# Optimization experiments

Hardware: AMD Instinct MI355X
Metric: run time of the kernel (lower is better)

## Reference

```python
import jax, jax.numpy as jnp
import numpy as np

N = 100000      # nodes
E = 3200000     # edges
H = 64          # node_hidden_dim
DIN = 15        # node_input_dim
DOUT = 12       # output_dim
NT = 5          # num_edge_type
G = 256         # graphs in batch
STEPS = 6       # num_step_prop


def setup_inputs() -> dict:
    key = jax.random.key(0)
    ks = jax.random.split(key, 24)
    s = 0.1
    n = lambda k, shp: jax.random.normal(k, shp, jnp.float32) * s
    return {
        "x": jax.random.normal(ks[0], (N, DIN), jnp.float32),
        "edge_index": jax.random.randint(ks[1], (2, E), 0, N, dtype=jnp.int32),
        "edge_attr": jax.random.randint(ks[2], (E,), 0, NT, dtype=jnp.int32),
        "batch": jnp.sort(jax.random.randint(ks[3], (N,), 0, G, dtype=jnp.int32)),
        "lin0_w": n(ks[4], (DIN, H)), "lin0_b": n(ks[5], (H,)),
        "edge_embed": n(ks[6], (NT, H * H)),
        "conv_bias": n(ks[7], (H,)),
        "gru_w_ih": n(ks[8], (H, 3 * H)), "gru_w_hh": n(ks[9], (H, 3 * H)),
        "gru_b_ih": n(ks[10], (3 * H,)), "gru_b_hh": n(ks[11], (3 * H,)),
        "i_w1": n(ks[12], (2 * H, H)), "i_b1": n(ks[13], (H,)),
        "i_w2": n(ks[14], (H, DOUT)), "i_b2": n(ks[15], (DOUT,)),
        "j_w1": n(ks[16], (H, H)), "j_b1": n(ks[17], (H,)),
        "j_w2": n(ks[18], (H, DOUT)), "j_b2": n(ks[19], (DOUT,)),
    }


def reference(x, edge_index, edge_attr, batch,
              lin0_w, lin0_b, edge_embed, conv_bias,
              gru_w_ih, gru_w_hh, gru_b_ih, gru_b_hh,
              i_w1, i_b1, i_w2, i_b2, j_w1, j_b1, j_w2, j_b2):
    src, dst = edge_index[0], edge_index[1]
    W_types = edge_embed.reshape(NT, H, H)  # per edge-type [H_in, H_out]

    # in-degree for mean aggregation (PyG: isolated nodes get 0)
    deg = jax.ops.segment_sum(jnp.ones((E,), x.dtype), dst, num_segments=N)
    deg = jnp.maximum(deg, 1.0)[:, None]

    out0 = jax.nn.relu(x @ lin0_w + lin0_b)
    out = out0
    h = out0

    for _ in range(STEPS):
        # NNConv: per-edge matmul m_e = x_src[e] @ W[type_e].
        # Only NT=5 edge types exist -> precompute all 5 transforms, then gather.
        T = jnp.einsum('nh,tho->nto', out, W_types)        # [N, NT, H]
        msg = T[src, edge_attr]                            # [E, H] gather
        agg = jax.ops.segment_sum(msg, dst, num_segments=N) / deg + conv_bias
        m = jax.nn.relu(agg)

        # GRU cell (torch gate order: r, z, n)
        gx = m @ gru_w_ih + gru_b_ih
        gh = h @ gru_w_hh + gru_b_hh
        xr, xz, xn = jnp.split(gx, 3, axis=1)
        hr, hz, hn = jnp.split(gh, 3, axis=1)
        r = jax.nn.sigmoid(xr + hr)
        z = jax.nn.sigmoid(xz + hz)
        nn_ = jnp.tanh(xn + r * hn)
        h = (1.0 - z) * nn_ + z * h
        out = h

    # gated readout
    i = jax.nn.sigmoid(
        jax.nn.sigmoid(jnp.concatenate([out, out0], axis=1) @ i_w1 + i_b1) @ i_w2 + i_b2)
    j = jax.nn.sigmoid(out @ j_w1 + j_b1) @ j_w2 + j_b2
    gated = i * j                                          # [N, DOUT]
    return jax.ops.segment_sum(gated, batch, num_segments=G)  # [G, DOUT]
```

## Files before the change

kernel.cpp:

```cpp
#include <hip/hip_runtime.h>
#include <hip/hip_bf16.h>

typedef __hip_bfloat16 bf16;
using short8 = __attribute__((ext_vector_type(8))) short;
using f32x4  = __attribute__((ext_vector_type(4))) float;
using f32x2  = __attribute__((ext_vector_type(2))) float;

#define MFMA16(a,b,c) __builtin_amdgcn_mfma_f32_16x16x32_bf16((a),(b),(c),0,0,0)
#define MAXBUCK 4096
#define SB 72
#define MSTR 72
#define SRCCAP 1024

__device__ __forceinline__ float b2f(bf16 v){ return __bfloat162float(v); }
__device__ __forceinline__ bf16  f2b(float v){ return __float2bfloat16(v); }
__device__ __forceinline__ float sigmf(float x){ return 1.f/(1.f+__expf(-x)); }
__device__ __forceinline__ float tanhfast(float x){
  x = fminf(fmaxf(x,-15.f),15.f);
  float e = __expf(2.f*x);
  return (e-1.f)/(e+1.f);
}
__device__ __forceinline__ short8 ld_frag(const bf16* p){
  return *reinterpret_cast<const short8*>(p);
}
__device__ __forceinline__ short f2bits(float f){
  unsigned u = __builtin_bit_cast(unsigned, f);
  unsigned r = (u + 0x7FFFu + ((u>>16)&1u)) >> 16;
  return (short)r;
}
__device__ __forceinline__ f32x2 up2(unsigned w){
  f32x2 r;
  r.x = __builtin_bit_cast(float, w<<16);
  r.y = __builtin_bit_cast(float, w & 0xFFFF0000u);
  return r;
}
__device__ __forceinline__ f32x2 pk_add(f32x2 a, f32x2 b){
  f32x2 d;
  asm("v_pk_add_f32 %0, %1, %2" : "=v"(d) : "v"(a), "v"(b));
  return d;
}
__device__ __forceinline__ unsigned cvtpk_bf16(float lo, float hi){
  unsigned r;
  asm("v_cvt_pk_bf16_f32 %0, %1, %2" : "=v"(r) : "v"(lo), "v"(hi));
  return r;
}


__global__ void k_sniff(const unsigned int* __restrict__ x, int* __restrict__ flag){
  int t = threadIdx.x;
  int good = 0;
  for (int i=t; i<4096; i+=256){
    unsigned w = x[i];
    unsigned e = (w>>23)&0xFFu;
    unsigned m = w & 0x7FFFFFFFu;
    if ((e>=100u && e<=150u) || m==0u) good++;
  }
  __shared__ int sm[256];
  sm[t]=good; __syncthreads();
  if (t==0){ int s=0; for (int k=0;k<256;k++) s+=sm[k]; *flag = (s>2048)?1:0; }
}

struct PtrPack { const void* p[17]; };

#define CAN_X     0
#define CAN_L0W   1500032
#define CAN_L0B   1500992
#define CAN_EE    1501056
#define CAN_CB    1521536
#define CAN_WIH   1521600
#define CAN_WHH   1533888
#define CAN_BIH   1546176
#define CAN_BHH   1546368
#define CAN_IW1   1546560
#define CAN_IB1   1554752
#define CAN_IW2   1554816
#define CAN_IB2   1555584
#define CAN_JW1   1555648
#define CAN_JB1   1559744
#define CAN_JW2   1559808
#define CAN_JB2   1560576
#define CAN_TOT   1560640

__global__ void k_canon(PtrPack pk, const int* __restrict__ flag, bf16* __restrict__ dst){
  static const int offs[17] = {CAN_X,CAN_L0W,CAN_L0B,CAN_EE,CAN_CB,CAN_WIH,CAN_WHH,
    CAN_BIH,CAN_BHH,CAN_IW1,CAN_IB1,CAN_IW2,CAN_IB2,CAN_JW1,CAN_JB1,CAN_JW2,CAN_JB2};
  static const int szs[17]  = {1500000,960,64,20480,64,12288,12288,192,192,8192,64,768,12,4096,64,768,12};
  int t = blockIdx.x*256+threadIdx.x;
  if (t >= CAN_TOT) return;
  int s = 0;
  #pragma unroll
  for (int k=1;k<17;k++) if (t >= offs[k]) s = k;
  int i = t - offs[s];
  float v = 0.f;
  if (i < szs[s]){
    if (*flag) v = ((const float*)pk.p[s])[i];
    else       v = b2f(((const bf16*)pk.p[s])[i]);
  }
  dst[t] = f2b(v);
}


__global__ __launch_bounds__(1024) void k_scan(const int* __restrict__ cnt, int n,
      int* __restrict__ ptr, int* __restrict__ cursor){
  __shared__ int ws[17];
  int tid = threadIdx.x, lane = tid&63, w = tid>>6;
  int run = 0;
  for (int base=0; base<n; base+=1024){
    int i = base + tid;
    int v = (i<n)? cnt[i] : 0;
    int incl = v;
    #pragma unroll
    for (int off=1; off<64; off<<=1){
      int t = __shfl_up(incl, off, 64);
      if (lane>=off) incl += t;
    }
    if (lane==63) ws[w] = incl;
    __syncthreads();
    if (tid==0){ int r=0; for (int k=0;k<16;k++){ int t=ws[k]; ws[k]=r; r+=t; } ws[16]=r; }
    __syncthreads();
    int excl = run + ws[w] + incl - v;
    if (i<n){
      ptr[i] = excl;
      if (cursor) cursor[i] = excl;
    }
    run += ws[16];
    __syncthreads();
  }
  if (tid==0) ptr[n] = run;
}

__global__ __launch_bounds__(256) void k_bcount(const int* __restrict__ dstv, int E_,
      int nb, int* __restrict__ bkt_cnt){
  __shared__ int lh[MAXBUCK];
  for (int i=threadIdx.x;i<nb;i+=256) lh[i]=0;
  __syncthreads();
  int base = blockIdx.x*4096;
  int end = min(base+4096, E_);
  for (int i=base+threadIdx.x; i<end; i+=256)
    atomicAdd(&lh[dstv[i]>>5], 1);
  __syncthreads();
  for (int i=threadIdx.x;i<nb;i+=256)
    if (lh[i]) atomicAdd(&bkt_cnt[i], lh[i]);
}

__global__ __launch_bounds__(256) void k_bscatter(const int* __restrict__ srcv,
      const int* __restrict__ dstv, const int* __restrict__ eav, int E_, int nb,
      int* __restrict__ cursor, unsigned int* __restrict__ bucketed){
  __shared__ int lh[MAXBUCK];
  __shared__ int lbase[MAXBUCK];
  for (int i=threadIdx.x;i<nb;i+=256) lh[i]=0;
  __syncthreads();
  int base = blockIdx.x*4096;
  int key[16]; int rnk[16]; unsigned pay[16];
  #pragma unroll
  for (int u=0;u<16;u++){
    int i = base + u*256 + threadIdx.x;
    bool valid = i < E_;
    int d = valid? dstv[i] : 0;
    int k = d>>5;
    key[u] = k;
    pay[u] = valid? (((unsigned)((d&31)*5 + eav[i]))<<17) | (unsigned)srcv[i] : 0u;
    rnk[u] = valid? atomicAdd(&lh[k],1) : 0;
  }
  __syncthreads();
  for (int i=threadIdx.x;i<nb;i+=256){
    int c = lh[i];
    lbase[i] = c? atomicAdd(&cursor[i], c) : 0;
  }
  __syncthreads();
  #pragma unroll
  for (int u=0;u<16;u++){
    int i = base + u*256 + threadIdx.x;
    if (i < E_) bucketed[lbase[key[u]] + rnk[u]] = pay[u];
  }
}

__global__ __launch_bounds__(256) void k_bsort(const unsigned int* __restrict__ bucketed,
      const int* __restrict__ bkt_ptr, int nb, int E_,
      int* __restrict__ kptr, int* __restrict__ sorted_src,
      unsigned char* __restrict__ kperm){
  __shared__ int cnt[160], sc[160], cur[160];
  int tid = threadIdx.x;
  int b = blockIdx.x;
  int s = bkt_ptr[b], e = bkt_ptr[b+1];
  if (tid<160) cnt[tid]=0;
  __syncthreads();
  for (int i=s+tid; i<e; i+=256) atomicAdd(&cnt[bucketed[i]>>17], 1);
  __syncthreads();
  if (tid<160) sc[tid]=cnt[tid];
  __syncthreads();
  #pragma unroll
  for (int off=1; off<160; off<<=1){
    int v = 0;
    if (tid<160 && tid>=off) v = sc[tid-off];
    __syncthreads();
    if (tid<160) sc[tid] += v;
    __syncthreads();
  }
  if (tid<160){
    int base = s + sc[tid] - cnt[tid];
    kptr[b*160+tid] = base;
    cur[tid] = base;
  }
  if (b==nb-1 && tid==0) kptr[(size_t)nb*160] = e;
  if (tid<160){
    int hbase = (tid<80)? 0 : 80;
    int me = cnt[tid];
    int r = 0;
    for (int j=0;j<80;j++){
      int jj = hbase+j;
      int cj = cnt[jj];
      r += (cj>me) || (cj==me && jj<tid);
    }
    kperm[((size_t)b*2 + (tid<80?0:1))*80 + r] = (unsigned char)(tid - hbase);
  }
  __syncthreads();
  for (int i=s+tid; i<e; i+=256){
    unsigned p = bucketed[i];
    int pos = atomicAdd(&cur[p>>17], 1);
    sorted_src[pos] = (int)(p & 0x1FFFFu);
  }
}

__global__ __launch_bounds__(256) void k_lin0(const bf16* __restrict__ x,
      const bf16* __restrict__ w, const bf16* __restrict__ b,
      bf16* __restrict__ out0, bf16* __restrict__ h, int N_){
  int idx = blockIdx.x*256+threadIdx.x;
  int n = idx>>6, o = idx&63;
  if (n>=N_) return;
  float acc = b2f(b[o]);
  #pragma unroll
  for (int k=0;k<15;k++) acc += b2f(x[n*15+k]) * b2f(w[k*64+o]);
  bf16 v = f2b(fmaxf(acc,0.f));
  out0[idx]=v; h[idx]=v;
}

__device__ __forceinline__ void d_swz(const unsigned short* src, int KS, int NC,
                                      unsigned short* dst, int nfrag, int t){
  if (t >= nfrag*64) return;
  int lane=t&63, frag=t>>6, cb=frag/KS, ks=frag%KS;
  int c = cb*16 + (lane&15);
  #pragma unroll
  for (int j=0;j<8;j++){
    int k = ks*32 + ((lane>>4)<<3) + j;
    dst[t*8+j] = (c<NC)? src[k*NC+c] : (unsigned short)0;
  }
}

__global__ __launch_bounds__(256) void k_prep(const bf16* __restrict__ ee,
      const bf16* __restrict__ wih, const bf16* __restrict__ whh,
      const bf16* __restrict__ iw1, const bf16* __restrict__ jw1,
      const bf16* __restrict__ iw2, const bf16* __restrict__ jw2,
      unsigned short* __restrict__ wall, unsigned short* __restrict__ wgru,
      unsigned short* __restrict__ wr1, unsigned short* __restrict__ wiw2s,
      unsigned short* __restrict__ wjw2s,
      const int* __restrict__ batch, int N_, int G_, int* __restrict__ gptr){
  int blk = blockIdx.x, tid = threadIdx.x;
  if (blk < 10){
    int t = blk*256+tid;
    if (t<2560){
      int lane=t&63, frag=t>>6, ct=frag/10, ks=frag%10;
      int c = ct*16 + (lane&15);
      #pragma unroll
      for (int j=0;j<8;j++){
        int k = ks*32 + ((lane>>4)<<3) + j;
        int tt = k>>6, kc = k&63;
        wall[t*8+j] = ((const unsigned short*)ee)[tt*4096 + kc*64 + c];
      }
    }
  } else if (blk < 16){
    d_swz((const unsigned short*)wih, 2, 192, wgru, 24, (blk-10)*256+tid);
  } else if (blk < 22){
    d_swz((const unsigned short*)whh, 2, 192, wgru+12288, 24, (blk-16)*256+tid);
  } else if (blk < 26){
    d_swz((const unsigned short*)iw1, 4, 64, wr1, 16, (blk-22)*256+tid);
  } else if (blk < 28){
    d_swz((const unsigned short*)jw1, 2, 64, wr1+8192, 8, (blk-26)*256+tid);
  } else if (blk == 28){
    d_swz((const unsigned short*)iw2, 2, 12, wiw2s, 2, tid);
  } else if (blk == 29){
    d_swz((const unsigned short*)jw2, 2, 12, wjw2s, 2, tid);
  } else {
    int g = (blk-30)*256+tid;
    if (g <= G_){
      int lo=0, hi=N_;
      while (lo<hi){ int mid=(lo+hi)>>1; if (batch[mid] < g) lo=mid+1; else hi=mid; }
      gptr[g]=lo;
    }
  }
}

__global__ __launch_bounds__(256,6) void k_step(const bf16* __restrict__ hin,
      bf16* __restrict__ hout,
      const int* __restrict__ sorted_src, const int* __restrict__ kptr,
      const unsigned char* __restrict__ kperm,
      const unsigned short* __restrict__ wall, const unsigned short* __restrict__ wgru,
      const bf16* __restrict__ conv_bias, const bf16* __restrict__ bih,
      const bf16* __restrict__ bhh, int N_){
  __shared__ unsigned short Sb[80*SB];
  __shared__ int kp[81];
  __shared__ unsigned char pm[80];
  __shared__ char ubuf[SRCCAP*4 + 32];
  int* srcL = (int*)ubuf;
  unsigned short* m_s = (unsigned short*)ubuf;
  int tid=threadIdx.x, lane=tid&63, w=tid>>6;
  int b=blockIdx.x;
  if (tid<81) kp[tid]=kptr[(size_t)b*80+tid];
  if (tid<80) pm[tid]=kperm[(size_t)b*80+tid];
  __syncthreads();
  int s0g = kp[0];
  int elen = kp[80]-s0g;
  int cap = (elen<=SRCCAP)? elen : 0;
  for (int i=tid;i<cap;i+=256) srcL[i]=sorted_src[s0g+i]<<7;
  __syncthreads();
  int g=lane>>3, c=lane&7;
  const int cOff = c<<4;
  const int sub4 = (g>>2)*4;
  const int pmk  = w*4 + (g&3);
  const int pm0  = w*4;
  const int sentB = N_<<7;
  const char* hbase = (const char*)hin;

  auto run_phase1 = [&](auto GET){
    int pC, stC, lenC, maxC;
    auto params = [&](int jo){
      int pp = pm[jo*16 + pmk];
      int p0 = pm[jo*16 + pm0];
      pC = pp;
      int k0 = kp[pp];
      stC  = k0 - s0g;
      lenC = kp[pp+1] - k0;
      maxC = kp[p0+1] - kp[p0];
    };
    auto finish = [&](int pS, f32x2 a01, f32x2 a23, f32x2 a45, f32x2 a67){
      float a[8] = {a01.x,a01.y,a23.x,a23.y,a45.x,a45.y,a67.x,a67.y};
      #pragma unroll
      for (int j=0;j<8;j++) a[j] += __shfl_xor(a[j], 32);
      if (g<4){
        uint4 v;
        v.x = cvtpk_bf16(a[0],a[1]);
        v.y = cvtpk_bf16(a[2],a[3]);
        v.z = cvtpk_bf16(a[4],a[5]);
        v.w = cvtpk_bf16(a[6],a[7]);
        *reinterpret_cast<uint4*>(&Sb[(size_t)pS*SB + c*8]) = v;
      }
    };
    uint4 A0,A1,A2,A3, B0,B1,B2,B3, T0,T1,T2,T3;
#define LD1(DST, st_, base_, off_, len_) do{                      \
      int idx_=(base_)+sub4+(off_);                               \
      int s_=GET((st_)+idx_);                                     \
      s_=(idx_<(len_))?s_:sentB;                                  \
      DST=*(const uint4*)(hbase+(unsigned)(s_+cOff)); }while(0)
#define ISSUE4(P, st_, base_, len_) do{                           \
      LD1(P##0,st_,base_,0,len_); LD1(P##1,st_,base_,1,len_);     \
      LD1(P##2,st_,base_,2,len_); LD1(P##3,st_,base_,3,len_); }while(0)
#define ACC1(V) do{                                               \
      a01=pk_add(a01,up2(V.x)); a23=pk_add(a23,up2(V.y));         \
      a45=pk_add(a45,up2(V.z)); a67=pk_add(a67,up2(V.w)); }while(0)
#define ACC4(P) do{ ACC1(P##0); ACC1(P##1); ACC1(P##2); ACC1(P##3); }while(0)
#define BODY(jo_, CUR, NXT) do{                                   \
      int pS=pC, stS=stC, lenS=lenC, maxS=maxC;                   \
      bool has2 = (maxS > 8);                                     \
      if (has2) ISSUE4(T, stS, 8, lenS);                          \
      if ((jo_) < 4){ params((jo_)+1); ISSUE4(NXT, stC, 0, lenC); } \
      f32x2 a01={0.f,0.f}, a23={0.f,0.f}, a45={0.f,0.f}, a67={0.f,0.f}; \
      ACC4(CUR);                                                  \
      if (has2){                                                  \
        ACC4(T);                                                  \
        for (int bse=16; bse<maxS; bse+=8){                       \
          ISSUE4(T, stS, bse, lenS);                              \
          ACC4(T);                                                \
        }                                                         \
      }                                                           \
      finish(pS, a01, a23, a45, a67); }while(0)
    params(0);
    ISSUE4(A, stC, 0, lenC);
    BODY(0, A, B);
    BODY(1, B, A);
    BODY(2, A, B);
    BODY(3, B, A);
    BODY(4, A, B);
#undef LD1
#undef ISSUE4
#undef ACC1
#undef ACC4
#undef BODY
  };
  if (cap) run_phase1([&](int rel){ return srcL[rel]; });
  else     run_phase1([&](int rel){ return sorted_src[s0g+rel]<<7; });
  __syncthreads();

  int q=lane>>4, mr=lane&15;
  {
    int ct = w;
    f32x4 acc={0.f,0.f,0.f,0.f};
    #pragma unroll
    for (int ks=0;ks<10;ks++){
      int k0 = ks*32 + q*8;
      int tt = k0>>6, ch = k0&63;
      short8 af = *reinterpret_cast<const short8*>(&Sb[(size_t)(mr*5+tt)*SB + ch]);
      short8 bfrag = *(const short8*)(wall + (size_t)((ct*10+ks)*64+lane)*8);
      acc = MFMA16(af, bfrag, acc);
    }
    int col = ct*16+mr;
    float bi = b2f(conv_bias[col]);
    #pragma unroll
    for (int r=0;r<4;r++){
      int nl = q*4+r;
      int deg = kp[nl*5+5]-kp[nl*5];
      float dv = 1.f/fmaxf((float)deg,1.f);
      m_s[nl*MSTR+col] = (unsigned short)f2bits(fmaxf(acc[r]*dv+bi,0.f));
    }
  }
  __syncthreads();

  {
    int cc = w;
    int na = b*16+mr; if (na>N_-1) na=N_-1;
    short8 am0 = *(const short8*)(&m_s[mr*MSTR + q*8]);
    short8 am1 = *(const short8*)(&m_s[mr*MSTR + 32 + q*8]);
    short8 ah0 = ld_frag(hin + (size_t)na*64 + q*8);
    short8 ah1 = ld_frag(hin + (size_t)na*64 + 32 + q*8);
    const short8* Bw = reinterpret_cast<const short8*>(wgru);
    f32x4 xr={0.f,0.f,0.f,0.f}, xz=xr, xn=xr, hr=xr, hz=xr, hn=xr;
    xr = MFMA16(am0, Bw[((cc  )*2+0)*64+lane], xr);
    xr = MFMA16(am1, Bw[((cc  )*2+1)*64+lane], xr);
    xz = MFMA16(am0, Bw[((cc+4)*2+0)*64+lane], xz);
    xz = MFMA16(am1, Bw[((cc+4)*2+1)*64+lane], xz);
    xn = MFMA16(am0, Bw[((cc+8)*2+0)*64+lane], xn);
    xn = MFMA16(am1, Bw[((cc+8)*2+1)*64+lane], xn);
    hr = MFMA16(ah0, Bw[(24+(cc  )*2+0)*64+lane], hr);
    hr = MFMA16(ah1, Bw[(24+(cc  )*2+1)*64+lane], hr);
    hz = MFMA16(ah0, Bw[(24+(cc+4)*2+0)*64+lane], hz);
    hz = MFMA16(ah1, Bw[(24+(cc+4)*2+1)*64+lane], hz);
    hn = MFMA16(ah0, Bw[(24+(cc+8)*2+0)*64+lane], hn);
    hn = MFMA16(ah1, Bw[(24+(cc+8)*2+1)*64+lane], hn);
    int col = cc*16+mr;
    float bxr=b2f(bih[col]), bxz=b2f(bih[col+64]), bxn=b2f(bih[col+128]);
    float bhr=b2f(bhh[col]), bhz=b2f(bhh[col+64]), bhn=b2f(bhh[col+128]);
    #pragma unroll
    for (int r=0;r<4;r++){
      int row = q*4+r;
      int n = b*16+row;
      if (n < N_){
        float rg = sigmf(xr[r]+bxr + hr[r]+bhr);
        float zg = sigmf(xz[r]+bxz + hz[r]+bhz);
        float ng = tanhfast(xn[r]+bxn + rg*(hn[r]+bhn));
        float ho = b2f(hin[(size_t)n*64+col]);
        hout[(size_t)n*64+col] = f2b((1.f-zg)*ng + zg*ho);
      }
    }
  }
}

__global__ __launch_bounds__(256) void k_read(const bf16* __restrict__ h, const bf16* __restrict__ out0,
      const unsigned short* __restrict__ W, const bf16* __restrict__ ib1, const bf16* __restrict__ jb1,
      const unsigned short* __restrict__ iw2swz, const unsigned short* __restrict__ jw2swz,
      const bf16* __restrict__ ib2, const bf16* __restrict__ jb2,
      float* __restrict__ gated, int N_){
  __shared__ unsigned short lds[12288];
  __shared__ unsigned short sbuf[64*72];
  __shared__ unsigned short tbuf[64*72];
  { const int* s=(const int*)W; int* d=(int*)lds;
    for (int i=threadIdx.x;i<6144;i+=256) d[i]=s[i]; }
  __syncthreads();
  int tid=threadIdx.x, lane=tid&63, w=tid>>6, q=lane>>4;
  int nb = blockIdx.x*64 + w*16;
  int ar = nb + (lane&15); if (ar>N_-1) ar=N_-1;
  short8 ah0 = ld_frag(h + (size_t)ar*64 + q*8),    ah1 = ld_frag(h + (size_t)ar*64 + 32 + q*8);
  short8 ao0 = ld_frag(out0 + (size_t)ar*64 + q*8), ao1 = ld_frag(out0 + (size_t)ar*64 + 32 + q*8);
  const short8* Bi = reinterpret_cast<const short8*>(lds);
  const short8* Bj = reinterpret_cast<const short8*>(lds + 8192);
  int colb = lane&15;
  for (int cb=0; cb<4; cb++){
    f32x4 ai = {0.f,0.f,0.f,0.f};
    ai = MFMA16(ah0, Bi[(cb*4+0)*64+lane], ai);
    ai = MFMA16(ah1, Bi[(cb*4+1)*64+lane], ai);
    ai = MFMA16(ao0, Bi[(cb*4+2)*64+lane], ai);
    ai = MFMA16(ao1, Bi[(cb*4+3)*64+lane], ai);
    f32x4 aj = {0.f,0.f,0.f,0.f};
    aj = MFMA16(ah0, Bj[(cb*2+0)*64+lane], aj);
    aj = MFMA16(ah1, Bj[(cb*2+1)*64+lane], aj);
    int col = cb*16 + colb;
    float bi=b2f(ib1[col]), bj=b2f(jb1[col]);
    #pragma unroll
    for (int r=0;r<4;r++){
      int lrow = w*16 + q*4 + r;
      sbuf[lrow*72+col] = (unsigned short)f2bits(sigmf(ai[r]+bi));
      tbuf[lrow*72+col] = (unsigned short)f2bits(sigmf(aj[r]+bj));
    }
  }
  __syncthreads();
  int mr = lane&15;
  short8 as0 = *(const short8*)(&sbuf[(w*16+mr)*72 + q*8]);
  short8 as1 = *(const short8*)(&sbuf[(w*16+mr)*72 + 32 + q*8]);
  short8 at0 = *(const short8*)(&tbuf[(w*16+mr)*72 + q*8]);
  short8 at1 = *(const short8*)(&tbuf[(w*16+mr)*72 + 32 + q*8]);
  const short8* Bi2 = reinterpret_cast<const short8*>(iw2swz);
  const short8* Bj2 = reinterpret_cast<const short8*>(jw2swz);
  f32x4 ai = {0.f,0.f,0.f,0.f};
  ai = MFMA16(as0, Bi2[lane], ai);
  ai = MFMA16(as1, Bi2[64+lane], ai);
  f32x4 aj = {0.f,0.f,0.f,0.f};
  aj = MFMA16(at0, Bj2[lane], aj);
  aj = MFMA16(at1, Bj2[64+lane], aj);
  int col = lane&15;
  if (col<12){
    float bi=b2f(ib2[col]), bj=b2f(jb2[col]);
    #pragma unroll
    for (int r=0;r<4;r++){
      int row = nb + q*4 + r;
      if (row < N_) gated[(size_t)row*12+col] = sigmf(ai[r]+bi)*(aj[r]+bj);
    }
  }
}

__global__ __launch_bounds__(256) void k_graphsum(const float* __restrict__ gated,
      const int* __restrict__ gptr, const int* __restrict__ flag, void* __restrict__ outp){
  int g = blockIdx.x;
  int s = gptr[g], e = gptr[g+1];
  int tid = threadIdx.x;
  int c = tid & 15, rg = tid >> 4;
  float acc = 0.f;
  if (c < 12)
    for (int row = s + rg; row < e; row += 16) acc += gated[(size_t)row*12 + c];
  __shared__ float sm[256];
  sm[tid] = acc;
  __syncthreads();
  if (rg == 0 && c < 12){
    float t = 0.f;
    for (int k=0;k<16;k++) t += sm[k*16 + c];
    if (*flag) ((float*)outp)[g*12 + c] = t;
    else       ((bf16*) outp)[g*12 + c] = f2b(t);
  }
}


extern "C" void kernel_launch(void* const* d_in, const int* in_sizes, int n_in,
                              void* d_out, int out_size, void* d_ws, size_t ws_size,
                              hipStream_t stream){
  const int*  ei    = (const int*) d_in[1];
  const int*  ea    = (const int*) d_in[2];
  const int*  batch = (const int*) d_in[3];

  const int N_ = in_sizes[3];
  const int E_ = in_sizes[2];
  const int G_ = out_size / 12;
  const int nb  = (N_ + 31) >> 5;
  const int nbs = (N_ + 15) >> 4;

  char* ws = (char*)d_ws;
  size_t off = 0;
  auto alloc = [&](size_t bytes)->size_t{
    size_t o = off; off += (bytes + 255) & ~(size_t)255; return o;
  };

  size_t oOut0   = alloc((size_t)N_*64*2);
  size_t oH0     = alloc((size_t)(N_+1)*64*2);
  size_t oH1     = alloc((size_t)(N_+1)*64*2);
  size_t oGated  = alloc((size_t)N_*12*4);
  size_t oBEdges = alloc((size_t)E_*4);
  size_t oSorted = alloc((size_t)E_*4 + 256);
  size_t oKptr   = alloc(((size_t)nb*160+2)*4);
  size_t oKperm  = alloc((size_t)nb*160);
  size_t oCanon  = alloc((size_t)CAN_TOT*2);
  size_t oCnt    = alloc((size_t)nb*4);
  size_t oBPtr   = alloc((size_t)(nb+1)*4);
  size_t oBCur   = alloc((size_t)nb*4);
  size_t oGptr   = alloc((size_t)(G_+1)*4);
  size_t oFlag   = alloc(256);
  size_t oWall   = alloc((size_t)20480*2);
  size_t oWgru   = alloc((size_t)24576*2);
  size_t oWr1    = alloc((size_t)12288*2);
  size_t oWiw2   = alloc((size_t)1024*2);
  size_t oWjw2   = alloc((size_t)1024*2);

  bf16*  out0    = (bf16*)(ws + oOut0);
  bf16*  h0      = (bf16*)(ws + oH0);
  bf16*  h1      = (bf16*)(ws + oH1);
  float* gated   = (float*)(ws + oGated);
  unsigned int* bucketed = (unsigned int*)(ws + oBEdges);
  int*   sorted_src = (int*)(ws + oSorted);
  int*   kptr    = (int*)(ws + oKptr);
  unsigned char* kperm = (unsigned char*)(ws + oKperm);
  bf16*  can     = (bf16*)(ws + oCanon);
  int*   bkt_cnt = (int*)(ws + oCnt);
  int*   bkt_ptr = (int*)(ws + oBPtr);
  int*   bkt_cur = (int*)(ws + oBCur);
  int*   gptr    = (int*)(ws + oGptr);
  int*   flag    = (int*)(ws + oFlag);
  unsigned short* wall  = (unsigned short*)(ws + oWall);
  unsigned short* wgru  = (unsigned short*)(ws + oWgru);
  unsigned short* wr1   = (unsigned short*)(ws + oWr1);
  unsigned short* wiw2s = (unsigned short*)(ws + oWiw2);
  unsigned short* wjw2s = (unsigned short*)(ws + oWjw2);

  const bf16* xC    = can + CAN_X;
  const bf16* l0wC  = can + CAN_L0W;
  const bf16* l0bC  = can + CAN_L0B;
  const bf16* eeC   = can + CAN_EE;
  const bf16* cbC   = can + CAN_CB;
  const bf16* wihC  = can + CAN_WIH;
  const bf16* whhC  = can + CAN_WHH;
  const bf16* bihC  = can + CAN_BIH;
  const bf16* bhhC  = can + CAN_BHH;
  const bf16* iw1C  = can + CAN_IW1;
  const bf16* ib1C  = can + CAN_IB1;
  const bf16* iw2C  = can + CAN_IW2;
  const bf16* ib2C  = can + CAN_IB2;
  const bf16* jw1C  = can + CAN_JW1;
  const bf16* jb1C  = can + CAN_JB1;
  const bf16* jw2C  = can + CAN_JW2;
  const bf16* jb2C  = can + CAN_JB2;

  PtrPack pk;
  pk.p[0]=d_in[0];  pk.p[1]=d_in[4];  pk.p[2]=d_in[5];  pk.p[3]=d_in[6];
  pk.p[4]=d_in[7];  pk.p[5]=d_in[8];  pk.p[6]=d_in[9];  pk.p[7]=d_in[10];
  pk.p[8]=d_in[11]; pk.p[9]=d_in[12]; pk.p[10]=d_in[13]; pk.p[11]=d_in[14];
  pk.p[12]=d_in[15]; pk.p[13]=d_in[16]; pk.p[14]=d_in[17]; pk.p[15]=d_in[18];
  pk.p[16]=d_in[19];

  const int gNw  = (N_+63)/64;
  const int gEc  = (E_+4095)/4096;

  k_sniff<<<1, 256, 0, stream>>>((const unsigned int*)d_in[0], flag);
  k_canon<<<(CAN_TOT+255)/256, 256, 0, stream>>>(pk, flag, can);
  hipMemsetAsync(ws + oCnt, 0, (size_t)nb*4, stream);
  hipMemsetAsync(ws + oH0 + (size_t)N_*128, 0, 128, stream);
  hipMemsetAsync(ws + oH1 + (size_t)N_*128, 0, 128, stream);
  k_bcount<<<gEc, 256, 0, stream>>>(ei + E_, E_, nb, bkt_cnt);
  k_scan<<<1, 1024, 0, stream>>>(bkt_cnt, nb, bkt_ptr, bkt_cur);
  k_bscatter<<<gEc, 256, 0, stream>>>(ei, ei + E_, ea, E_, nb, bkt_cur, bucketed);
  k_bsort<<<nb, 256, 0, stream>>>(bucketed, bkt_ptr, nb, E_, kptr, sorted_src, kperm);
  k_lin0<<<(N_*64+255)/256, 256, 0, stream>>>(xC, l0wC, l0bC, out0, h0, N_);
  k_prep<<<32, 256, 0, stream>>>(eeC, wihC, whhC, iw1C, jw1C, iw2C, jw2C,
                                 wall, wgru, wr1, wiw2s, wjw2s, batch, N_, G_, gptr);

  bf16* hb[2] = {h0, h1};
  for (int step = 0; step < 6; ++step){
    k_step<<<nbs, 256, 0, stream>>>(hb[step&1], hb[(step+1)&1], sorted_src, kptr, kperm,
                                    wall, wgru, cbC, bihC, bhhC, N_);
  }
  bf16* hfin = hb[0];

  k_read<<<gNw, 256, 0, stream>>>(hfin, out0, wr1, ib1C, jb1C, wiw2s, wjw2s,
                                  ib2C, jb2C, gated, N_);
  k_graphsum<<<G_, 256, 0, stream>>>(gated, gptr, flag, d_out);
}
```

Measured before the change: 704.4 us.

## Use inline-asm gathers with explicit vmcnt waits and raise occupancy to 8

Replaces the compiler-generated gather loads in the edge-aggregation phase with inline global_load_dwordx4 instructions and explicit s_waitcnt vmcnt counters. It drops the separate T register set so only one batch is prefetched ahead, and raises launch bounds from 6 to 8 waves per SIMD. The goal is to cut VGPR use so more waves can hide gather latency, while controlling how loads and waits overlap. In exchange, each block has less memory-level parallelism for nodes with high in-degree, because the tail loop now waits with vmcnt(0) on every iteration.

Result: slower. 720.7 us (+2.3%).

```diff
diff --git a/kernel.cpp b/kernel.cpp
--- a/kernel.cpp
+++ b/kernel.cpp
@@ -290,7 +290,7 @@
   }
 }
 
-__global__ __launch_bounds__(256,6) void k_step(const bf16* __restrict__ hin,
+__global__ __launch_bounds__(256,8) void k_step(const bf16* __restrict__ hin,
       bf16* __restrict__ hout,
       const int* __restrict__ sorted_src, const int* __restrict__ kptr,
       const unsigned char* __restrict__ kperm,
@@ -319,7 +319,7 @@
   const int pmk  = w*4 + (g&3);
   const int pm0  = w*4;
   const int sentB = N_<<7;
-  const char* hbase = (const char*)hin;
+  const void* hvoid = (const void*)hin;
 
   auto run_phase1 = [&](auto GET){
     int pC, stC, lenC, maxC;
@@ -345,33 +345,34 @@
         *reinterpret_cast<uint4*>(&Sb[(size_t)pS*SB + c*8]) = v;
       }
     };
-    uint4 A0,A1,A2,A3, B0,B1,B2,B3, T0,T1,T2,T3;
-#define LD1(DST, st_, base_, off_, len_) do{                      \
-      int idx_=(base_)+sub4+(off_);                               \
-      int s_=GET((st_)+idx_);                                     \
-      s_=(idx_<(len_))?s_:sentB;                                  \
-      DST=*(const uint4*)(hbase+(unsigned)(s_+cOff)); }while(0)
-#define ISSUE4(P, st_, base_, len_) do{                           \
-      LD1(P##0,st_,base_,0,len_); LD1(P##1,st_,base_,1,len_);     \
-      LD1(P##2,st_,base_,2,len_); LD1(P##3,st_,base_,3,len_); }while(0)
-#define ACC1(V) do{                                               \
-      a01=pk_add(a01,up2(V.x)); a23=pk_add(a23,up2(V.y));         \
+    uint4 A0,A1,A2,A3, B0,B1,B2,B3;
+#define GLD(DST, st_, base_, off_, len_) do{                         \
+      int idx_=(base_)+sub4+(off_);                                  \
+      int s_=GET((st_)+idx_);                                        \
+      unsigned voff_=(unsigned)(((idx_<(len_))?s_:sentB)+cOff);      \
+      asm volatile("global_load_dwordx4 %0, %1, %2"                  \
+        : "=&v"(DST) : "v"(voff_), "s"(hvoid) : "memory"); }while(0)
+#define ISSUE4(P, st_, base_, len_) do{                              \
+      GLD(P##0,st_,base_,0,len_); GLD(P##1,st_,base_,1,len_);        \
+      GLD(P##2,st_,base_,2,len_); GLD(P##3,st_,base_,3,len_); }while(0)
+#define WAITV(N) do{ asm volatile("s_waitcnt vmcnt(" #N ")" ::: "memory"); \
+      __builtin_amdgcn_sched_barrier(0); }while(0)
+#define ACC1(V) do{                                                  \
+      a01=pk_add(a01,up2(V.x)); a23=pk_add(a23,up2(V.y));            \
       a45=pk_add(a45,up2(V.z)); a67=pk_add(a67,up2(V.w)); }while(0)
 #define ACC4(P) do{ ACC1(P##0); ACC1(P##1); ACC1(P##2); ACC1(P##3); }while(0)
-#define BODY(jo_, CUR, NXT) do{                                   \
-      int pS=pC, stS=stC, lenS=lenC, maxS=maxC;                   \
-      bool has2 = (maxS > 8);                                     \
-      if (has2) ISSUE4(T, stS, 8, lenS);                          \
-      if ((jo_) < 4){ params((jo_)+1); ISSUE4(NXT, stC, 0, lenC); } \
+#define BODY(jo_, CUR, NXT) do{                                      \
+      int pS=pC, stS=stC, lenS=lenC, maxS=maxC;                      \
+      if ((jo_) < 4){ params((jo_)+1); ISSUE4(NXT, stC, 0, lenC);    \
+                      WAITV(4); }                                    \
+      else          { WAITV(0); }                                    \
       f32x2 a01={0.f,0.f}, a23={0.f,0.f}, a45={0.f,0.f}, a67={0.f,0.f}; \
-      ACC4(CUR);                                                  \
-      if (has2){                                                  \
-        ACC4(T);                                                  \
-        for (int bse=16; bse<maxS; bse+=8){                       \
-          ISSUE4(T, stS, bse, lenS);                              \
-          ACC4(T);                                                \
-        }                                                         \
-      }                                                           \
+      ACC4(CUR);                                                     \
+      for (int bse=8; bse<maxS; bse+=8){                             \
+        ISSUE4(CUR, stS, bse, lenS);                                 \
+        WAITV(0);                                                    \
+        ACC4(CUR);                                                   \
+      }                                                              \
       finish(pS, a01, a23, a45, a67); }while(0)
     params(0);
     ISSUE4(A, stC, 0, lenC);
@@ -380,8 +381,9 @@
     BODY(2, A, B);
     BODY(3, B, A);
     BODY(4, A, B);
-#undef LD1
+#undef GLD
 #undef ISSUE4
+#undef WAITV
 #undef ACC1
 #undef ACC4
 #undef BODY
```
